# Performance work log

Measured on AMD Instinct MI355X. Metric: run time of the kernel, lower is better.

## Reference

```python
import jax, jax.numpy as jnp
import numpy as np

N_NODES = 50000
N_EDGES = 800000
IN_CH = 512
HIDDEN = 512


def setup_inputs() -> dict:
    key = jax.random.key(0)
    k1, k2, k3, k4 = jax.random.split(key, 4)
    x = jax.random.normal(k1, (N_NODES, IN_CH), dtype=jnp.float32)
    edge_index = jax.random.randint(k2, (2, N_EDGES), 0, N_NODES, dtype=jnp.int64)
    # Glorot-style scaling for weights
    W1 = jax.random.normal(k3, (IN_CH, HIDDEN), dtype=jnp.float32) / np.sqrt(IN_CH)
    b1 = jnp.zeros((HIDDEN,), dtype=jnp.float32)
    W2 = jax.random.normal(k4, (HIDDEN, 1), dtype=jnp.float32) / np.sqrt(HIDDEN)
    b2 = jnp.zeros((1,), dtype=jnp.float32)
    return {"x": x, "edge_index": edge_index, "W1": W1, "b1": b1, "W2": W2, "b2": b2}


def _gcn_conv(x, edge_index, W, b):
    """PyG GCNConv: add self-loops, symmetric D^{-1/2}(A+I)D^{-1/2} normalization."""
    N = x.shape[0]
    xw = x @ W                                   # [N, out]
    row, col = edge_index[0], edge_index[1]      # source -> target
    # degree on target nodes, +1 for the self-loop
    deg = jax.ops.segment_sum(jnp.ones_like(col, dtype=xw.dtype), col, num_segments=N) + 1.0
    dis = jax.lax.rsqrt(deg)                     # deg^{-1/2}, [N]
    norm = dis[row] * dis[col]                   # [E]
    agg = jax.ops.segment_sum(norm[:, None] * xw[row], col, num_segments=N)
    agg = agg + (dis * dis)[:, None] * xw        # self-loop contribution
    return agg + b


def reference(x, edge_index, W1, b1, W2, b2):
    h = jax.nn.relu(_gcn_conv(x, edge_index, W1, b1))
    # dropout in eval mode (training=False) -> identity
    out = _gcn_conv(h, edge_index, W2, b2)
    return out.squeeze(-1)                       # [N]
```

## Files before the change

kernel.cpp:

```cpp
#include <hip/hip_runtime.h>

#define IN_CH 512
#define SCAN_BLK 1024

typedef _Float16 f16x8 __attribute__((ext_vector_type(8)));
typedef float f32x4 __attribute__((ext_vector_type(4)));

__device__ __forceinline__ void gload_lds16(const void* g, void* l) {
    __builtin_amdgcn_global_load_lds(
        (const __attribute__((address_space(1))) unsigned int*)g,
        (__attribute__((address_space(3))) unsigned int*)l, 16, 0, 0);
}

__global__ __launch_bounds__(SCAN_BLK) void k_psum(const int* __restrict__ deg,
                                                   int* __restrict__ bsum, int N) {
    __shared__ int red[SCAN_BLK / 64];
    int i = blockIdx.x * SCAN_BLK + threadIdx.x;
    int v = (i < N) ? deg[i] : 0;
#pragma unroll
    for (int off = 32; off > 0; off >>= 1) v += __shfl_down(v, off);
    if ((threadIdx.x & 63) == 0) red[threadIdx.x >> 6] = v;
    __syncthreads();
    if (threadIdx.x == 0) {
        int s = 0;
#pragma unroll
        for (int u = 0; u < SCAN_BLK / 64; ++u) s += red[u];
        bsum[blockIdx.x] = s;
    }
}

__global__ __launch_bounds__(SCAN_BLK) void k_write(const int* __restrict__ deg,
                                                    const int* __restrict__ bsum,
                                                    int* __restrict__ rp,
                                                    float* __restrict__ dis,
                                                    int* __restrict__ cursor, int N) {
    __shared__ int sums[SCAN_BLK];
    __shared__ int boff_s, tot_s;
    int t = threadIdx.x;
    if (t < 64) {
        int v = (t < (int)gridDim.x) ? bsum[t] : 0;
        int pre = (t < (int)blockIdx.x) ? v : 0;
        int a = pre, b = v;
#pragma unroll
        for (int off = 32; off > 0; off >>= 1) {
            a += __shfl_down(a, off);
            b += __shfl_down(b, off);
        }
        if (t == 0) { boff_s = a; tot_s = b; }
    }
    int i = blockIdx.x * SCAN_BLK + t;
    int d = (i < N) ? deg[i] : 0;
    sums[t] = d;
    __syncthreads();
    for (int off = 1; off < SCAN_BLK; off <<= 1) {
        int u = (t >= off) ? sums[t - off] : 0;
        __syncthreads();
        sums[t] += u;
        __syncthreads();
    }
    if (i < N) {
        rp[i] = boff_s + sums[t] - d;
        dis[i] = rsqrtf((float)d + 1.0f);
        cursor[i] = 0;
    }
    if (blockIdx.x == gridDim.x - 1 && t == 0) rp[N] = tot_s;
}

__global__ void k_fill(const int* __restrict__ ei, const int* __restrict__ rp,
                       int* __restrict__ cursor, int* __restrict__ csrc,
                       int E, int N) {
    int e = blockIdx.x * blockDim.x + threadIdx.x;
    if (e < E) {
        int s = ei[e];
        int d = ei[E + e];
        if ((unsigned)s < (unsigned)N && (unsigned)d < (unsigned)N) {
            int pos = atomicAdd(&cursor[d], 1);
            csrc[rp[d] + pos] = s;
        }
    }
}

__global__ __launch_bounds__(256) void k_cvt_w(const float* __restrict__ W1,
                                               _Float16* __restrict__ W1t) {
    __shared__ float tile[32][33];
    const int bk = blockIdx.x * 32, bn = blockIdx.y * 32;
    const int tx = threadIdx.x & 31, ty = threadIdx.x >> 5;
#pragma unroll
    for (int p = 0; p < 4; ++p)
        tile[ty + p * 8][tx] = W1[(size_t)(bk + ty + p * 8) * 512 + bn + tx];
    __syncthreads();
#pragma unroll
    for (int p = 0; p < 4; ++p)
        W1t[(size_t)(bn + ty + p * 8) * 512 + bk + tx] = (_Float16)tile[tx][ty + p * 8];
}

__global__ __launch_bounds__(256) void k_merged(const float* __restrict__ A,
                                                const _Float16* __restrict__ Bt,
                                                _Float16* __restrict__ C,
                                                int Nrows, int nbm,
                                                const int* __restrict__ col,
                                                int* __restrict__ deg, int E, int N) {
    __shared__ __align__(16) _Float16 As[128 * 64];
    __shared__ __align__(16) _Float16 Bs[128 * 64];
    const int nwg = nbm * 4;

    if ((int)blockIdx.x >= nwg) {
        int e = ((int)blockIdx.x - nwg) * 256 + threadIdx.x;
        if (e < E) {
            int d = col[e];
            if ((unsigned)d < (unsigned)N) atomicAdd(&deg[d], 1);
        }
        return;
    }

    const int t = threadIdx.x;
    const int lane = t & 63, w = t >> 6;
    const int wm = w >> 1, wn = w & 1;

    const int q = nwg >> 3, r = nwg & 7;
    const int xcd = blockIdx.x & 7, within = blockIdx.x >> 3;
    const int wg = (xcd < r ? xcd * (q + 1) : r * (q + 1) + (xcd - r) * q) + within;
    const int bm = (wg >> 2) * 128, bn = (wg & 3) * 128;

    const int rr = lane & 15, kg = lane >> 4;
    const int lrow = lane >> 3, lcol = (lane & 7) * 8;
    const int arow = t >> 3, acol = (t & 7) * 8;

    f32x4 acc[4][4];
#pragma unroll
    for (int i = 0; i < 4; ++i)
#pragma unroll
        for (int j = 0; j < 4; ++j) acc[i][j] = (f32x4)0.0f;

    for (int k0 = 0; k0 < 512; k0 += 64) {
#pragma unroll
        for (int p = 0; p < 4; ++p) {
            const int row = p * 32 + w * 8 + lrow;
            gload_lds16(Bt + (size_t)(bn + row) * 512 + k0 + lcol,
                        Bs + (p * 32 + w * 8) * 64);
        }
#pragma unroll
        for (int p = 0; p < 4; ++p) {
            int grow = bm + p * 32 + arow;
            if (grow >= Nrows) grow = Nrows - 1;
            const float* gp = A + (size_t)grow * 512 + k0 + acol;
            float4 u0 = *(const float4*)gp;
            float4 u1 = *(const float4*)(gp + 4);
            f16x8 o;
            o[0] = (_Float16)u0.x; o[1] = (_Float16)u0.y;
            o[2] = (_Float16)u0.z; o[3] = (_Float16)u0.w;
            o[4] = (_Float16)u1.x; o[5] = (_Float16)u1.y;
            o[6] = (_Float16)u1.z; o[7] = (_Float16)u1.w;
            *(f16x8*)(As + ((p * 32 + arow) * 64 + acol)) = o;
        }
        __syncthreads();
#pragma unroll
        for (int kk = 0; kk < 2; ++kk) {
            f16x8 a[4], b[4];
#pragma unroll
            for (int i = 0; i < 4; ++i)
                a[i] = *(const f16x8*)(As + (wm * 64 + i * 16 + rr) * 64 + kk * 32 + kg * 8);
#pragma unroll
            for (int j = 0; j < 4; ++j)
                b[j] = *(const f16x8*)(Bs + (wn * 64 + j * 16 + rr) * 64 + kk * 32 + kg * 8);
#pragma unroll
            for (int i = 0; i < 4; ++i)
#pragma unroll
                for (int j = 0; j < 4; ++j)
                    acc[i][j] = __builtin_amdgcn_mfma_f32_16x16x32_f16(a[i], b[j], acc[i][j], 0, 0, 0);
        }
        __syncthreads();
    }

#pragma unroll
    for (int i = 0; i < 4; ++i)
#pragma unroll
        for (int j = 0; j < 4; ++j)
#pragma unroll
            for (int reg = 0; reg < 4; ++reg) {
                int m = bm + wm * 64 + i * 16 + kg * 4 + reg;
                int n = bn + wn * 64 + j * 16 + rr;
                C[(size_t)m * 512 + n] = (_Float16)acc[i][j][reg];
            }
}

__global__ __launch_bounds__(256) void k_agg(const _Float16* __restrict__ y,
                                             const float* __restrict__ dis,
                                             const int* __restrict__ rp,
                                             const int* __restrict__ csrc,
                                             const float* __restrict__ b1,
                                             const float* __restrict__ W2,
                                             float* __restrict__ z, int N) {
    const int n = blockIdx.x * 4 + (threadIdx.x >> 6);
    if (n >= N) return;
    const int l = threadIdx.x & 63;

    const float d1 = dis[n];
    f16x8 self = *(const f16x8*)(y + (size_t)n * 512 + l * 8);
    float acc[8];
#pragma unroll
    for (int c = 0; c < 8; ++c) acc[c] = d1 * (float)self[c];

    int j = rp[n], jend = rp[n + 1];
    for (; j + 8 <= jend; j += 8) {
        int s[8]; float wt[8]; f16x8 v[8];
#pragma unroll
        for (int u = 0; u < 8; ++u) s[u] = csrc[j + u];
#pragma unroll
        for (int u = 0; u < 8; ++u) wt[u] = dis[s[u]];
#pragma unroll
        for (int u = 0; u < 8; ++u)
            v[u] = *(const f16x8*)(y + (size_t)s[u] * 512 + l * 8);
#pragma unroll
        for (int u = 0; u < 8; ++u)
#pragma unroll
            for (int c = 0; c < 8; ++c) acc[c] += wt[u] * (float)v[u][c];
    }
    for (; j + 2 <= jend; j += 2) {
        int s0 = csrc[j], s1 = csrc[j + 1];
        float w0 = dis[s0], w1 = dis[s1];
        f16x8 v0 = *(const f16x8*)(y + (size_t)s0 * 512 + l * 8);
        f16x8 v1 = *(const f16x8*)(y + (size_t)s1 * 512 + l * 8);
#pragma unroll
        for (int c = 0; c < 8; ++c) acc[c] += w0 * (float)v0[c] + w1 * (float)v1[c];
    }
    if (j < jend) {
        int s0 = csrc[j];
        float w0 = dis[s0];
        f16x8 v0 = *(const f16x8*)(y + (size_t)s0 * 512 + l * 8);
#pragma unroll
        for (int c = 0; c < 8; ++c) acc[c] += w0 * (float)v0[c];
    }

    float4 bb0 = *(const float4*)(b1 + l * 8);
    float4 bb1 = *(const float4*)(b1 + l * 8 + 4);
    float4 w20 = *(const float4*)(W2 + l * 8);
    float4 w21 = *(const float4*)(W2 + l * 8 + 4);
    float bbv[8] = {bb0.x, bb0.y, bb0.z, bb0.w, bb1.x, bb1.y, bb1.z, bb1.w};
    float w2v[8] = {w20.x, w20.y, w20.z, w20.w, w21.x, w21.y, w21.z, w21.w};
    float p = 0.0f;
#pragma unroll
    for (int c = 0; c < 8; ++c) {
        float h = fmaxf(acc[c] * d1 + bbv[c], 0.0f);
        p += h * w2v[c];
    }
#pragma unroll
    for (int off = 32; off > 0; off >>= 1) p += __shfl_down(p, off);
    if (l == 0) z[n] = d1 * p;
}

__global__ void k_out(const float* __restrict__ z, const float* __restrict__ dis,
                      const int* __restrict__ rp, const int* __restrict__ csrc,
                      const float* __restrict__ b2, float* __restrict__ out, int N) {
    int n = blockIdx.x * blockDim.x + threadIdx.x;
    if (n >= N) return;
    float acc = z[n];
    int j = rp[n], jend = rp[n + 1];
    for (; j + 4 <= jend; j += 4) {
        float a0 = z[csrc[j]];
        float a1 = z[csrc[j + 1]];
        float a2 = z[csrc[j + 2]];
        float a3 = z[csrc[j + 3]];
        acc += (a0 + a1) + (a2 + a3);
    }
    for (; j < jend; ++j) acc += z[csrc[j]];
    out[n] = dis[n] * acc + b2[0];
}

extern "C" void kernel_launch(void* const* d_in, const int* in_sizes, int n_in,
                              void* d_out, int out_size, void* d_ws, size_t ws_size,
                              hipStream_t stream) {
    const float* x  = (const float*)d_in[0];
    const int*   ei = (const int*)d_in[1];
    const float* W1 = (const float*)d_in[2];
    const float* b1 = (const float*)d_in[3];
    const float* W2 = (const float*)d_in[4];
    const float* b2 = (const float*)d_in[5];
    float* out = (float*)d_out;

    const int N = in_sizes[0] / IN_CH;
    const int E = in_sizes[1] / 2;
    const int nbm = (N + 127) / 128;
    const int M2 = nbm * 128;
    const int NB = (N + SCAN_BLK - 1) / SCAN_BLK;
    const int DEGB = (E + 255) / 256;

    char* ws = (char*)d_ws;
    size_t off = 0;
    auto alloc = [&](size_t bytes) {
        char* p = ws + off;
        off += (bytes + 255) & ~(size_t)255;
        return p;
    };
    _Float16* y   = (_Float16*)alloc((size_t)M2 * 512 * sizeof(_Float16));
    _Float16* W1t = (_Float16*)alloc((size_t)512 * 512 * sizeof(_Float16));
    int*   deg    = (int*)alloc((size_t)N * sizeof(int));
    float* dis    = (float*)alloc((size_t)N * sizeof(float));
    int*   rp     = (int*)alloc((size_t)(N + 1) * sizeof(int));
    int*   cursor = (int*)alloc((size_t)N * sizeof(int));
    int*   csrc   = (int*)alloc((size_t)E * sizeof(int));
    float* z      = (float*)alloc((size_t)N * sizeof(float));
    int*   bsum   = (int*)alloc((size_t)64 * sizeof(int));

    hipMemsetAsync(deg, 0, (size_t)N * sizeof(int), stream);

    k_cvt_w<<<dim3(16, 16), 256, 0, stream>>>(W1, W1t);
    k_merged<<<nbm * 4 + DEGB, 256, 0, stream>>>(x, W1t, y, N, nbm,
                                                 ei + E, deg, E, N);
    k_psum<<<NB, SCAN_BLK, 0, stream>>>(deg, bsum, N);
    k_write<<<NB, SCAN_BLK, 0, stream>>>(deg, bsum, rp, dis, cursor, N);
    k_fill<<<(E + 255) / 256, 256, 0, stream>>>(ei, rp, cursor, csrc, E, N);
    k_agg<<<(N + 3) / 4, 256, 0, stream>>>(y, dis, rp, csrc, b1, W2, z, N);
    k_out<<<(N + 255) / 256, 256, 0, stream>>>(z, dis, rp, csrc, b2, out, N);
}
```

Before: 265.5 us.

## Split aggregation across eight channel slices with partial-sum reduction kernel

The aggregation kernel now splits the 512 channels into eight 64-channel slices, each handled by its own block, so each lane loads one fp16 element per neighbor instead of a 16-byte vector. Per-slice partial dot products with W2 go to an 8xN buffer, and a new kernel sums them before the output aggregation. The aim is more parallelism and more waves in flight to hide gather latency. In exchange, each gather becomes a 2-byte per-lane load (128 bytes per wave), index and degree-scale reads repeat eight times, and an extra launch plus extra buffer traffic are added.

```diff
diff --git a/kernel.cpp b/kernel.cpp
--- a/kernel.cpp
+++ b/kernel.cpp
@@ -190,63 +190,45 @@
                                              const int* __restrict__ csrc,
                                              const float* __restrict__ b1,
                                              const float* __restrict__ W2,
-                                             float* __restrict__ z, int N) {
-    const int n = blockIdx.x * 4 + (threadIdx.x >> 6);
+                                             float* __restrict__ zp, int N) {
+    const int s = blockIdx.x & 7;
+    const int n = (blockIdx.x >> 3) * 4 + (threadIdx.x >> 6);
     if (n >= N) return;
     const int l = threadIdx.x & 63;
+    const int c = s * 64 + l;
 
     const float d1 = dis[n];
-    f16x8 self = *(const f16x8*)(y + (size_t)n * 512 + l * 8);
-    float acc[8];
-#pragma unroll
-    for (int c = 0; c < 8; ++c) acc[c] = d1 * (float)self[c];
+    float acc = d1 * (float)y[(size_t)n * 512 + c];
 
     int j = rp[n], jend = rp[n + 1];
-    for (; j + 8 <= jend; j += 8) {
-        int s[8]; float wt[8]; f16x8 v[8];
-#pragma unroll
-        for (int u = 0; u < 8; ++u) s[u] = csrc[j + u];
-#pragma unroll
-        for (int u = 0; u < 8; ++u) wt[u] = dis[s[u]];
-#pragma unroll
-        for (int u = 0; u < 8; ++u)
-            v[u] = *(const f16x8*)(y + (size_t)s[u] * 512 + l * 8);
-#pragma unroll
-        for (int u = 0; u < 8; ++u)
-#pragma unroll
-            for (int c = 0; c < 8; ++c) acc[c] += wt[u] * (float)v[u][c];
-    }
-    for (; j + 2 <= jend; j += 2) {
-        int s0 = csrc[j], s1 = csrc[j + 1];
-        float w0 = dis[s0], w1 = dis[s1];
-        f16x8 v0 = *(const f16x8*)(y + (size_t)s0 * 512 + l * 8);
-        f16x8 v1 = *(const f16x8*)(y + (size_t)s1 * 512 + l * 8);
-#pragma unroll
-        for (int c = 0; c < 8; ++c) acc[c] += w0 * (float)v0[c] + w1 * (float)v1[c];
-    }
-    if (j < jend) {
+    for (; j + 4 <= jend; j += 4) {
+        int s0 = csrc[j], s1 = csrc[j + 1], s2 = csrc[j + 2], s3 = csrc[j + 3];
+        float w0 = dis[s0], w1 = dis[s1], w2 = dis[s2], w3 = dis[s3];
+        float v0 = (float)y[(size_t)s0 * 512 + c];
+        float v1 = (float)y[(size_t)s1 * 512 + c];
+        float v2 = (float)y[(size_t)s2 * 512 + c];
+        float v3 = (float)y[(size_t)s3 * 512 + c];
+        acc += (w0 * v0 + w1 * v1) + (w2 * v2 + w3 * v3);
+    }
+    for (; j < jend; ++j) {
         int s0 = csrc[j];
-        float w0 = dis[s0];
-        f16x8 v0 = *(const f16x8*)(y + (size_t)s0 * 512 + l * 8);
-#pragma unroll
-        for (int c = 0; c < 8; ++c) acc[c] += w0 * (float)v0[c];
-    }
-
-    float4 bb0 = *(const float4*)(b1 + l * 8);
-    float4 bb1 = *(const float4*)(b1 + l * 8 + 4);
-    float4 w20 = *(const float4*)(W2 + l * 8);
-    float4 w21 = *(const float4*)(W2 + l * 8 + 4);
-    float bbv[8] = {bb0.x, bb0.y, bb0.z, bb0.w, bb1.x, bb1.y, bb1.z, bb1.w};
-    float w2v[8] = {w20.x, w20.y, w20.z, w20.w, w21.x, w21.y, w21.z, w21.w};
-    float p = 0.0f;
-#pragma unroll
-    for (int c = 0; c < 8; ++c) {
-        float h = fmaxf(acc[c] * d1 + bbv[c], 0.0f);
-        p += h * w2v[c];
-    }
+        acc += dis[s0] * (float)y[(size_t)s0 * 512 + c];
+    }
+
+    float h = fmaxf(acc * d1 + b1[c], 0.0f);
+    float p = h * W2[c];
 #pragma unroll
     for (int off = 32; off > 0; off >>= 1) p += __shfl_down(p, off);
-    if (l == 0) z[n] = d1 * p;
+    if (l == 0) zp[(size_t)s * N + n] = d1 * p;
+}
+
+__global__ void k_zred(const float* __restrict__ zp, float* __restrict__ zsum, int N) {
+    int n = blockIdx.x * blockDim.x + threadIdx.x;
+    if (n >= N) return;
+    float a = 0.0f;
+#pragma unroll
+    for (int s = 0; s < 8; ++s) a += zp[(size_t)s * N + n];
+    zsum[n] = a;
 }
 
 __global__ void k_out(const float* __restrict__ z, const float* __restrict__ dis,
@@ -299,7 +281,8 @@
     int*   rp     = (int*)alloc((size_t)(N + 1) * sizeof(int));
     int*   cursor = (int*)alloc((size_t)N * sizeof(int));
     int*   csrc   = (int*)alloc((size_t)E * sizeof(int));
-    float* z      = (float*)alloc((size_t)N * sizeof(float));
+    float* zp     = (float*)alloc((size_t)8 * N * sizeof(float));
+    float* zsum   = (float*)alloc((size_t)N * sizeof(float));
     int*   bsum   = (int*)alloc((size_t)64 * sizeof(int));
 
     hipMemsetAsync(deg, 0, (size_t)N * sizeof(int), stream);
@@ -310,6 +293,7 @@
     k_psum<<<NB, SCAN_BLK, 0, stream>>>(deg, bsum, N);
     k_write<<<NB, SCAN_BLK, 0, stream>>>(deg, bsum, rp, dis, cursor, N);
     k_fill<<<(E + 255) / 256, 256, 0, stream>>>(ei, rp, cursor, csrc, E, N);
-    k_agg<<<(N + 3) / 4, 256, 0, stream>>>(y, dis, rp, csrc, b1, W2, z, N);
-    k_out<<<(N + 255) / 256, 256, 0, stream>>>(z, dis, rp, csrc, b2, out, N);
-}
+    k_agg<<<((N + 3) / 4) * 8, 256, 0, stream>>>(y, dis, rp, csrc, b1, W2, zp, N);
+    k_zred<<<(N + 255) / 256, 256, 0, stream>>>(zp, zsum, N);
+    k_out<<<(N + 255) / 256, 256, 0, stream>>>(zsum, dis, rp, csrc, b2, out, N);
+}
```

Result: slower. 393.4 us (+48.2%).

## Rebalance kernel merging: pair degree count with weight convert, fill with GEMM

Applied to the files above, without the earlier changes.

The degree-count atomics now run in the same launch as the W1 transpose/convert. The CSR fill work runs inside the GEMM launch as leading blocks, which removes the standalone fill kernel. The intent is to drop a launch and hide the atomic-heavy fill behind the GEMM instead of running it serially after the scan. The fill grid is padded to a multiple of 8 so the GEMM blocks keep their XCD-aware mapping. The risk is that the GEMM now starts after the scan kernels instead of overlapping the degree count.

```diff
diff --git a/kernel.cpp b/kernel.cpp
--- a/kernel.cpp
+++ b/kernel.cpp
@@ -10,6 +10,30 @@
     __builtin_amdgcn_global_load_lds(
         (const __attribute__((address_space(1))) unsigned int*)g,
         (__attribute__((address_space(3))) unsigned int*)l, 16, 0, 0);
+}
+
+__global__ __launch_bounds__(256) void k_merged1(const float* __restrict__ W1,
+                                                 _Float16* __restrict__ W1t,
+                                                 const int* __restrict__ col,
+                                                 int* __restrict__ deg, int E, int N) {
+    __shared__ float tile[32][33];
+    if ((int)blockIdx.x >= 256) {
+        int e = ((int)blockIdx.x - 256) * 256 + threadIdx.x;
+        if (e < E) {
+            int d = col[e];
+            if ((unsigned)d < (unsigned)N) atomicAdd(&deg[d], 1);
+        }
+        return;
+    }
+    const int bk = (blockIdx.x & 15) * 32, bn = (blockIdx.x >> 4) * 32;
+    const int tx = threadIdx.x & 31, ty = threadIdx.x >> 5;
+#pragma unroll
+    for (int p = 0; p < 4; ++p)
+        tile[ty + p * 8][tx] = W1[(size_t)(bk + ty + p * 8) * 512 + bn + tx];
+    __syncthreads();
+#pragma unroll
+    for (int p = 0; p < 4; ++p)
+        W1t[(size_t)(bn + ty + p * 8) * 512 + bk + tx] = (_Float16)tile[tx][ty + p * 8];
 }
 
 __global__ __launch_bounds__(SCAN_BLK) void k_psum(const int* __restrict__ deg,
@@ -66,59 +90,39 @@
     if (blockIdx.x == gridDim.x - 1 && t == 0) rp[N] = tot_s;
 }
 
-__global__ void k_fill(const int* __restrict__ ei, const int* __restrict__ rp,
-                       int* __restrict__ cursor, int* __restrict__ csrc,
-                       int E, int N) {
-    int e = blockIdx.x * blockDim.x + threadIdx.x;
-    if (e < E) {
-        int s = ei[e];
-        int d = ei[E + e];
-        if ((unsigned)s < (unsigned)N && (unsigned)d < (unsigned)N) {
-            int pos = atomicAdd(&cursor[d], 1);
-            csrc[rp[d] + pos] = s;
-        }
-    }
-}
-
-__global__ __launch_bounds__(256) void k_cvt_w(const float* __restrict__ W1,
-                                               _Float16* __restrict__ W1t) {
-    __shared__ float tile[32][33];
-    const int bk = blockIdx.x * 32, bn = blockIdx.y * 32;
-    const int tx = threadIdx.x & 31, ty = threadIdx.x >> 5;
-#pragma unroll
-    for (int p = 0; p < 4; ++p)
-        tile[ty + p * 8][tx] = W1[(size_t)(bk + ty + p * 8) * 512 + bn + tx];
-    __syncthreads();
-#pragma unroll
-    for (int p = 0; p < 4; ++p)
-        W1t[(size_t)(bn + ty + p * 8) * 512 + bk + tx] = (_Float16)tile[tx][ty + p * 8];
-}
-
-__global__ __launch_bounds__(256) void k_merged(const float* __restrict__ A,
-                                                const _Float16* __restrict__ Bt,
-                                                _Float16* __restrict__ C,
-                                                int Nrows, int nbm,
-                                                const int* __restrict__ col,
-                                                int* __restrict__ deg, int E, int N) {
+__global__ __launch_bounds__(256) void k_merged2(const float* __restrict__ A,
+                                                 const _Float16* __restrict__ Bt,
+                                                 _Float16* __restrict__ C,
+                                                 int Nrows, int nbm, int fillb,
+                                                 const int* __restrict__ ei,
+                                                 const int* __restrict__ rp,
+                                                 int* __restrict__ cursor,
+                                                 int* __restrict__ csrc,
+                                                 int E, int N) {
     __shared__ __align__(16) _Float16 As[128 * 64];
     __shared__ __align__(16) _Float16 Bs[128 * 64];
+
+    if ((int)blockIdx.x < fillb) {
+        int e = (int)blockIdx.x * 256 + threadIdx.x;
+        if (e < E) {
+            int s = ei[e];
+            int d = ei[E + e];
+            if ((unsigned)s < (unsigned)N && (unsigned)d < (unsigned)N) {
+                int pos = atomicAdd(&cursor[d], 1);
+                csrc[rp[d] + pos] = s;
+            }
+        }
+        return;
+    }
+
+    const int g = (int)blockIdx.x - fillb;
     const int nwg = nbm * 4;
-
-    if ((int)blockIdx.x >= nwg) {
-        int e = ((int)blockIdx.x - nwg) * 256 + threadIdx.x;
-        if (e < E) {
-            int d = col[e];
-            if ((unsigned)d < (unsigned)N) atomicAdd(&deg[d], 1);
-        }
-        return;
-    }
-
     const int t = threadIdx.x;
     const int lane = t & 63, w = t >> 6;
     const int wm = w >> 1, wn = w & 1;
 
     const int q = nwg >> 3, r = nwg & 7;
-    const int xcd = blockIdx.x & 7, within = blockIdx.x >> 3;
+    const int xcd = g & 7, within = g >> 3;
     const int wg = (xcd < r ? xcd * (q + 1) : r * (q + 1) + (xcd - r) * q) + within;
     const int bm = (wg >> 2) * 128, bn = (wg & 3) * 128;
 
@@ -283,7 +287,8 @@
     const int nbm = (N + 127) / 128;
     const int M2 = nbm * 128;
     const int NB = (N + SCAN_BLK - 1) / SCAN_BLK;
-    const int DEGB = (E + 255) / 256;
+    const int DEGB  = (E + 255) / 256;
+    const int FILLB = ((DEGB + 7) / 8) * 8;
 
     char* ws = (char*)d_ws;
     size_t off = 0;
@@ -304,12 +309,11 @@
 
     hipMemsetAsync(deg, 0, (size_t)N * sizeof(int), stream);
 
-    k_cvt_w<<<dim3(16, 16), 256, 0, stream>>>(W1, W1t);
-    k_merged<<<nbm * 4 + DEGB, 256, 0, stream>>>(x, W1t, y, N, nbm,
-                                                 ei + E, deg, E, N);
+    k_merged1<<<256 + DEGB, 256, 0, stream>>>(W1, W1t, ei + E, deg, E, N);
     k_psum<<<NB, SCAN_BLK, 0, stream>>>(deg, bsum, N);
     k_write<<<NB, SCAN_BLK, 0, stream>>>(deg, bsum, rp, dis, cursor, N);
-    k_fill<<<(E + 255) / 256, 256, 0, stream>>>(ei, rp, cursor, csrc, E, N);
+    k_merged2<<<FILLB + nbm * 4, 256, 0, stream>>>(x, W1t, y, N, nbm, FILLB,
+                                                   ei, rp, cursor, csrc, E, N);
     k_agg<<<(N + 3) / 4, 256, 0, stream>>>(y, dis, rp, csrc, b1, W2, z, N);
     k_out<<<(N + 255) / 256, 256, 0, stream>>>(z, dis, rp, csrc, b2, out, N);
 }
```

Measured after the change: 263.7 us. Within noise of the previous version (-0.7%).
